# Performance work log

Hardware: AMD Instinct MI355X
Metric: run time of the kernel (lower is better)

## Reference

```python
import jax, jax.numpy as jnp
import numpy as np

# Product fuzzy logic (embed-wise):
#   bin_xnor(a,b)    = a*b + (1-a)*(1-b)
#   implies(a,b)     = 1 - a*(1-b)
#   conjoin(x,dim)   = prod(x, dim)
#   bin_conjoin(a,b) = a*b
#   disjoin(x,dim)   = 1 - prod(1-x, dim)

B, IN_F, HID_F, OUT_F, E = 128, 256, 512, 128, 8

def setup_inputs() -> dict:
    key = jax.random.key(0)
    k0, k1, k2, k3 = jax.random.split(key, 4)
    return {
        "input": jax.random.uniform(k0, (B, IN_F, E), dtype=jnp.float32),
        "conj_weights": jax.random.uniform(k1, (IN_F, HID_F, E), dtype=jnp.float32),
        "conj_signs": jax.random.uniform(k2, (IN_F, HID_F, E), dtype=jnp.float32),
        "disj_weights": jax.random.uniform(k3, (HID_F, OUT_F, E), dtype=jnp.float32),
    }

def reference(input, conj_weights, conj_signs, disj_weights):
    # --- EmbedSignedConjunction ---
    x = input[:, :, None, :]                      # [B, in, 1, E]
    xnor = x * conj_signs + (1.0 - x) * (1.0 - conj_signs)   # [B, in, hid, E]
    impl = 1.0 - conj_weights * (1.0 - xnor)      # implies(w, xnor)
    h = jnp.prod(impl, axis=1)                    # conjoin over in -> [B, hid, E]

    # --- EmbedUnsignedDisjunction ---
    hh = h[:, :, None, :]                         # [B, hid, 1, E]
    conj = disj_weights * hh                      # bin_conjoin -> [B, hid, out, E]
    out = 1.0 - jnp.prod(1.0 - conj, axis=1)      # disjoin over hid -> [B, out, E]
    return out
```

## Files before the change

kernel.cpp:

```cpp
#include <hip/hip_runtime.h>


#define LD4(p) (*(const float4*)(p))

static __device__ __forceinline__ float4 f4mul(float4 a, float4 b) {
    return make_float4(a.x*b.x, a.y*b.y, a.z*b.z, a.w*b.w);
}
static __device__ __forceinline__ float4 f4fma(float4 a, float4 b, float4 c) {
    return make_float4(fmaf(a.x,b.x,c.x), fmaf(a.y,b.y,c.y),
                       fmaf(a.z,b.z,c.z), fmaf(a.w,b.w,c.w));
}
static __device__ __forceinline__ float4 f4nfma1(float4 d, float4 h) {
    return make_float4(fmaf(-d.x,h.x,1.0f), fmaf(-d.y,h.y,1.0f),
                       fmaf(-d.z,h.z,1.0f), fmaf(-d.w,h.w,1.0f));
}

__global__ __launch_bounds__(256, 4) void k_stage1(
    const float* __restrict__ in,
    const float* __restrict__ cw,
    const float* __restrict__ cs,
    float* __restrict__ P1)
{
    __shared__ float lds[4096];
    const int t    = threadIdx.x;
    const int lane = t & 63;
    const int kc   = t >> 6;
    const int eh   = lane & 1;
    const int hl   = lane >> 1;
    const int bid  = blockIdx.x;
    const int hg   = (bid & 3) | (((bid >> 3) & 3) << 2);
    const int ks   = ((bid >> 2) & 1) | (((bid >> 5) & 3) << 1);
    const int bg   = bid >> 7;
    const int b0   = bg * 8;
    const int h    = hg * 32 + hl;
    const int e0   = eh * 4;

    {
        float4* xs4 = (float4*)lds;
        #pragma unroll
        for (int k = 0; k < 2; ++k) {
            const int f4  = t + k * 256;
            const int b   = f4 >> 6;
            const int col = f4 & 63;
            xs4[f4] = LD4(in + (b0 + b) * 2048 + ks * 256 + col * 4);
        }
    }
    __syncthreads();

    const int i0 = ks * 32 + kc * 8;
    const float* pw = cw + i0 * 4096 + h * 8 + e0;
    const float* ps = cs + i0 * 4096 + h * 8 + e0;
    const float* xbase = lds + kc * 64 + e0;

    float4 acc[8];
    #pragma unroll
    for (int b = 0; b < 8; ++b) acc[b] = make_float4(1.f, 1.f, 1.f, 1.f);

    #pragma unroll
    for (int ii = 0; ii < 8; ++ii) {
        const float4 wv = LD4(pw);
        const float4 sv = LD4(ps);
        pw += 4096; ps += 4096;
        const float4 p  = f4mul(wv, sv);
        const float4 A  = make_float4(1.f - p.x, 1.f - p.y, 1.f - p.z, 1.f - p.w);
        const float4 Bv = make_float4(fmaf(2.f, p.x, -wv.x), fmaf(2.f, p.y, -wv.y),
                                      fmaf(2.f, p.z, -wv.z), fmaf(2.f, p.w, -wv.w));
        #pragma unroll
        for (int b = 0; b < 8; ++b) {
            const float4 xv = LD4(xbase + b * 256 + ii * 8);
            acc[b] = f4mul(acc[b], f4fma(xv, Bv, A));
        }
    }

    __syncthreads();
    #pragma unroll
    for (int phase = 0; phase < 2; ++phase) {
        if (phase) __syncthreads();
        #pragma unroll
        for (int j = 0; j < 4; ++j)
            *(float4*)&lds[kc * 1024 + j * 256 + hl * 8 + e0] = acc[phase * 4 + j];
        __syncthreads();
        {
            const int o4 = t * 4;
            float4 m = LD4(&lds[o4]);
            #pragma unroll
            for (int c = 1; c < 4; ++c) m = f4mul(m, LD4(&lds[c * 1024 + o4]));
            const int j   = o4 >> 8;
            const int hl2 = (o4 >> 3) & 31;
            const int eq  = o4 & 7;
            *(float4*)(P1 + ks * 524288 + (hg * 32 + hl2) * 1024
                          + (b0 + phase * 4 + j) * 8 + eq) = m;
        }
    }
}

__global__ __launch_bounds__(256, 4) void k_stage2(
    const float* __restrict__ dw,
    const float* __restrict__ P1,
    float* __restrict__ P2)
{
    __shared__ float lds[4096];
    const int t    = threadIdx.x;
    const int lane = t & 63;
    const int kc   = t >> 6;
    const int eh   = lane & 1;
    const int ol   = lane >> 1;
    const int ks   = blockIdx.x & 15;
    const int og   = (blockIdx.x >> 4) & 3;
    const int bg   = blockIdx.x >> 6;
    const int b0   = bg * 8;
    const int o    = og * 32 + ol;
    const int e0   = eh * 4;
    const int h0   = ks * 32;

    {
        float4* ht4 = (float4*)lds;
        #pragma unroll
        for (int k = 0; k < 2; ++k) {
            const int f4  = t + k * 256;
            const int hl  = f4 >> 4;
            const int rem = f4 & 15;
            const float* q = P1 + (h0 + hl) * 1024 + b0 * 8 + rem * 4;
            float4 m = LD4(q);
            #pragma unroll
            for (int c = 1; c < 8; ++c) m = f4mul(m, LD4(q + c * 524288));
            ht4[f4] = m;
        }
    }
    __syncthreads();

    const float* pd = dw + (h0 + kc * 8) * 1024 + o * 8 + e0;
    const float* hbase = lds + kc * 512 + e0;

    float4 acc[8];
    #pragma unroll
    for (int b = 0; b < 8; ++b) acc[b] = make_float4(1.f, 1.f, 1.f, 1.f);

    #pragma unroll
    for (int ii = 0; ii < 8; ++ii) {
        const float4 dv = LD4(pd);
        pd += 1024;
        #pragma unroll
        for (int b = 0; b < 8; ++b) {
            const float4 hv = LD4(hbase + ii * 64 + b * 8);
            acc[b] = f4mul(acc[b], f4nfma1(dv, hv));
        }
    }

    __syncthreads();
    #pragma unroll
    for (int phase = 0; phase < 2; ++phase) {
        if (phase) __syncthreads();
        #pragma unroll
        for (int j = 0; j < 4; ++j)
            *(float4*)&lds[kc * 1024 + j * 256 + ol * 8 + e0] = acc[phase * 4 + j];
        __syncthreads();
        {
            const int o4 = t * 4;
            float4 m = LD4(&lds[o4]);
            #pragma unroll
            for (int c = 1; c < 4; ++c) m = f4mul(m, LD4(&lds[c * 1024 + o4]));
            const int j   = o4 >> 8;
            const int ol2 = (o4 >> 3) & 31;
            const int eq  = o4 & 7;
            *(float4*)(P2 + ks * 131072 + (b0 + phase * 4 + j) * 1024
                          + (og * 32 + ol2) * 8 + eq) = m;
        }
    }
}

__global__ __launch_bounds__(256, 4) void k_comb2(
    const float* __restrict__ P2,
    float* __restrict__ out)
{
    const int idx4 = blockIdx.x * 256 + threadIdx.x;
    float4 m = LD4(P2 + idx4 * 4);
    #pragma unroll
    for (int c = 1; c < 16; ++c)
        m = f4mul(m, LD4(P2 + c * 131072 + idx4 * 4));
    const float4 r = make_float4(1.f - m.x, 1.f - m.y, 1.f - m.z, 1.f - m.w);
    *(float4*)(out + idx4 * 4) = r;
}

extern "C" void kernel_launch(void* const* d_in, const int* in_sizes, int n_in,
                              void* d_out, int out_size, void* d_ws, size_t ws_size,
                              hipStream_t stream)
{
    const float* in = (const float*)d_in[0];
    const float* cw = (const float*)d_in[1];
    const float* cs = (const float*)d_in[2];
    const float* dw = (const float*)d_in[3];
    float* outp = (float*)d_out;
    float* P1   = (float*)d_ws;
    float* P2   = (float*)d_ws + 4194304;

    k_stage1<<<2048, 256, 0, stream>>>(in, cw, cs, P1);
    k_stage2<<<1024, 256, 0, stream>>>(dw, P1, P2);
    k_comb2<<<128, 256, 0, stream>>>(P2, outp);
}
```

Measured before the change: 88.63 us.

## Retile stage1 to 16 batches and 2 embeds per thread

Stage1 now gives each thread 2 embed lanes (float2) and 16 batch rows instead of 4 lanes and 8 rows, with 16 hidden units per block instead of 32. Each weight/sign load is reused across twice as many batch rows, cutting global traffic per useful flop, and more x data is staged in LDS per block. The cross-warp LDS reduction and the block-index decode are rewritten to match. In exchange, global and LDS accesses use narrower 8-byte loads and stores.

```diff
diff --git a/kernel.cpp b/kernel.cpp
--- a/kernel.cpp
+++ b/kernel.cpp
@@ -2,13 +2,10 @@
 
 
 #define LD4(p) (*(const float4*)(p))
+#define LD2(p) (*(const float2*)(p))
 
 static __device__ __forceinline__ float4 f4mul(float4 a, float4 b) {
     return make_float4(a.x*b.x, a.y*b.y, a.z*b.z, a.w*b.w);
-}
-static __device__ __forceinline__ float4 f4fma(float4 a, float4 b, float4 c) {
-    return make_float4(fmaf(a.x,b.x,c.x), fmaf(a.y,b.y,c.y),
-                       fmaf(a.z,b.z,c.z), fmaf(a.w,b.w,c.w));
 }
 static __device__ __forceinline__ float4 f4nfma1(float4 d, float4 h) {
     return make_float4(fmaf(-d.x,h.x,1.0f), fmaf(-d.y,h.y,1.0f),
@@ -25,20 +22,20 @@
     const int t    = threadIdx.x;
     const int lane = t & 63;
     const int kc   = t >> 6;
-    const int eh   = lane & 1;
-    const int hl   = lane >> 1;
+    const int eQ   = lane & 3;
+    const int hl   = lane >> 2;
     const int bid  = blockIdx.x;
-    const int hg   = (bid & 3) | (((bid >> 3) & 3) << 2);
-    const int ks   = ((bid >> 2) & 1) | (((bid >> 5) & 3) << 1);
-    const int bg   = bid >> 7;
-    const int b0   = bg * 8;
-    const int h    = hg * 32 + hl;
-    const int e0   = eh * 4;
+    const int hg   = (bid & 3) | (((bid >> 5) & 7) << 2);
+    const int ks   = ((bid >> 2) & 1) | (((bid >> 3) & 3) << 1);
+    const int bg   = bid >> 8;
+    const int b0   = bg * 16;
+    const int h    = hg * 16 + hl;
+    const int e0   = eQ * 2;
 
     {
         float4* xs4 = (float4*)lds;
         #pragma unroll
-        for (int k = 0; k < 2; ++k) {
+        for (int k = 0; k < 4; ++k) {
             const int f4  = t + k * 256;
             const int b   = f4 >> 6;
             const int col = f4 & 63;
@@ -50,46 +47,52 @@
     const int i0 = ks * 32 + kc * 8;
     const float* pw = cw + i0 * 4096 + h * 8 + e0;
     const float* ps = cs + i0 * 4096 + h * 8 + e0;
-    const float* xbase = lds + kc * 64 + e0;
-
-    float4 acc[8];
-    #pragma unroll
-    for (int b = 0; b < 8; ++b) acc[b] = make_float4(1.f, 1.f, 1.f, 1.f);
+    const float* xb = lds + kc * 64 + e0;
+
+    float2 acc[16];
+    #pragma unroll
+    for (int b = 0; b < 16; ++b) acc[b] = make_float2(1.f, 1.f);
 
     #pragma unroll
     for (int ii = 0; ii < 8; ++ii) {
-        const float4 wv = LD4(pw);
-        const float4 sv = LD4(ps);
+        const float2 w2 = LD2(pw);
+        const float2 s2 = LD2(ps);
         pw += 4096; ps += 4096;
-        const float4 p  = f4mul(wv, sv);
-        const float4 A  = make_float4(1.f - p.x, 1.f - p.y, 1.f - p.z, 1.f - p.w);
-        const float4 Bv = make_float4(fmaf(2.f, p.x, -wv.x), fmaf(2.f, p.y, -wv.y),
-                                      fmaf(2.f, p.z, -wv.z), fmaf(2.f, p.w, -wv.w));
-        #pragma unroll
-        for (int b = 0; b < 8; ++b) {
-            const float4 xv = LD4(xbase + b * 256 + ii * 8);
-            acc[b] = f4mul(acc[b], f4fma(xv, Bv, A));
-        }
-    }
-
-    __syncthreads();
+        const float2 p  = make_float2(w2.x * s2.x, w2.y * s2.y);
+        const float2 A  = make_float2(1.f - p.x, 1.f - p.y);
+        const float2 Bv = make_float2(fmaf(2.f, p.x, -w2.x),
+                                      fmaf(2.f, p.y, -w2.y));
+        #pragma unroll
+        for (int b = 0; b < 16; ++b) {
+            const float2 xv = LD2(xb + b * 256 + ii * 8);
+            acc[b].x *= fmaf(xv.x, Bv.x, A.x);
+            acc[b].y *= fmaf(xv.y, Bv.y, A.y);
+        }
+    }
+
+    float2* cmb = (float2*)lds;
     #pragma unroll
     for (int phase = 0; phase < 2; ++phase) {
-        if (phase) __syncthreads();
-        #pragma unroll
-        for (int j = 0; j < 4; ++j)
-            *(float4*)&lds[kc * 1024 + j * 256 + hl * 8 + e0] = acc[phase * 4 + j];
         __syncthreads();
-        {
-            const int o4 = t * 4;
-            float4 m = LD4(&lds[o4]);
+        #pragma unroll
+        for (int b = 0; b < 8; ++b)
+            cmb[kc * 512 + b * 64 + lane] = acc[phase * 8 + b];
+        __syncthreads();
+        #pragma unroll
+        for (int r = 0; r < 2; ++r) {
+            const int s = t * 2 + r;
+            float2 m = cmb[s];
             #pragma unroll
-            for (int c = 1; c < 4; ++c) m = f4mul(m, LD4(&lds[c * 1024 + o4]));
-            const int j   = o4 >> 8;
-            const int hl2 = (o4 >> 3) & 31;
-            const int eq  = o4 & 7;
-            *(float4*)(P1 + ks * 524288 + (hg * 32 + hl2) * 1024
-                          + (b0 + phase * 4 + j) * 8 + eq) = m;
+            for (int c = 1; c < 4; ++c) {
+                const float2 v = cmb[c * 512 + s];
+                m.x *= v.x; m.y *= v.y;
+            }
+            const int b   = s >> 6;
+            const int rem = s & 63;
+            const int hs  = rem >> 2;
+            const int eq  = rem & 3;
+            *(float2*)(P1 + ks * 524288 + (hg * 16 + hs) * 1024
+                          + (b0 + phase * 8 + b) * 8 + eq * 2) = m;
         }
     }
 }
```

Measured after the change: 91.13 us. +2.8%, slower.
